# Performance work log

Hardware: AMD Instinct MI355X
Metric: run time of the kernel (lower is better)

Reference implementation:

```python
import jax, jax.numpy as jnp
import numpy as np

B, C_IN, H, W = 4, 64, 512, 512
C_OUT = 64


def _box_sum(x):
    """3x3 box sum with zero padding == applying (A + I) for the 8-connected grid.
    x: [B, H, W, C] -> [B, H, W, C]
    """
    b, h, w, c = x.shape
    xp = jnp.pad(x, ((0, 0), (1, 1), (1, 1), (0, 0)))
    out = jnp.zeros_like(x)
    for i in range(3):
        for j in range(3):
            out = out + xp[:, i:i + h, j:j + w, :]
    return out


def setup_inputs() -> dict:
    key = jax.random.key(0)
    k1, k2 = jax.random.split(key)
    x = jax.random.normal(k1, (B, C_IN, H, W), dtype=jnp.float32)
    weight = jax.random.normal(k2, (1, C_IN, C_OUT), dtype=jnp.float32)
    return {"x": x, "weight": weight}


def reference(x, weight):
    b, c, h, w = x.shape
    o = weight.shape[-1]
    # x.permute(0,2,3,1).reshape(B, H*W, C) -> keep as [B,H,W,C] grid
    x1 = jnp.transpose(x, (0, 2, 3, 1))
    # xw = x1 @ weight  (weight has leading broadcast dim of 1)
    xw = jnp.einsum('bhwc,co->bhwo', x1, weight[0])
    # Normalized adjacency D^{-1/2}(A+I)D^{-1/2} as a 3x3 stencil:
    # deg = number of 8-neighbors + self-loop (9 interior, 6 edge, 4 corner)
    deg = _box_sum(jnp.ones((1, h, w, 1), dtype=x.dtype))
    dinv = 1.0 / jnp.sqrt(deg)  # no isolated nodes on a grid
    y = dinv * _box_sum(dinv * xw)  # [B,H,W,O]
    # out.permute(0,2,1).reshape(B, O, W, H); with H==W this equals plain NCHW
    out = jnp.transpose(y, (0, 3, 1, 2)).reshape(b, o, w, h)
    return out
```

## Files before the change

kernel.cpp:

```cpp
#include <hip/hip_runtime.h>

#define HH 512
#define WWID 512
#define CIN 64
#define COUT 64
#define TH 8
#define TW 32

__device__ __forceinline__ float edge_rsqrt(int y, int n) {
  int r = 1 + (y > 0 ? 1 : 0) + (y < n - 1 ? 1 : 0);
  return __frsqrt_rn((float)r);
}

__global__ __launch_bounds__(256, 4)
void gcn_fused(const float* __restrict__ x, const float* __restrict__ wgt,
               float* __restrict__ out) {
  __shared__ __align__(16) float ts[4][TH * TW];

  const int t  = threadIdx.x;
  const int g  = t & 63;
  const int og = __builtin_amdgcn_readfirstlane(t >> 6);
  const int b  = blockIdx.z;
  const int h0 = blockIdx.y * TH;
  const int w0 = blockIdx.x * TW;
  const int row = g >> 3;
  const int cg  = g & 7;
  const int h = h0 + row;
  const int w = w0 + cg * 4;

  float srh[3]; int hi[3];
#pragma unroll
  for (int i = 0; i < 3; ++i) {
    int y = h - 1 + i;
    bool v = (y >= 0) && (y < HH);
    srh[i] = v ? edge_rsqrt(y, HH) : 0.0f;
    hi[i] = v ? y : h;
  }
  float srw[6];
#pragma unroll
  for (int j = 0; j < 6; ++j) {
    int xw = w - 1 + j;
    bool v = (xw >= 0) && (xw < WWID);
    srw[j] = v ? edge_rsqrt(xw, WWID) : 0.0f;
  }
  const int wl = (w > 0) ? (w - 1) : w;
  const int wr = (w + 4 < WWID) ? (w + 4) : w;
  const float dp0 = srh[1] * srw[1];
  const float dp1 = srh[1] * srw[2];
  const float dp2 = srh[1] * srw[3];
  const float dp3 = srh[1] * srw[4];

  float4 acc[16];
#pragma unroll
  for (int j = 0; j < 16; ++j) acc[j] = make_float4(0.f, 0.f, 0.f, 0.f);

  const size_t plane = (size_t)HH * WWID;
  const float* xb = x + (size_t)b * CIN * plane;

  float lv[3], rv[3]; float4 mv[3];
  {
    const float* xp = xb + (size_t)og * plane;
#pragma unroll
    for (int i = 0; i < 3; ++i) {
      const float* rp = xp + (size_t)hi[i] * WWID;
      lv[i] = rp[wl];
      mv[i] = *(const float4*)(rp + w);
      rv[i] = rp[wr];
    }
  }

  for (int ci = 0; ci < 16; ++ci) {
    float t0 = 0.f, t1 = 0.f, t2 = 0.f, t3 = 0.f;
#pragma unroll
    for (int i = 0; i < 3; ++i) {
      float m0 = lv[i] * srw[0];
      float m1 = mv[i].x * srw[1];
      float m2 = mv[i].y * srw[2];
      float m3 = mv[i].z * srw[3];
      float m4 = mv[i].w * srw[4];
      float m5 = rv[i] * srw[5];
      t0 += srh[i] * (m0 + m1 + m2);
      t1 += srh[i] * (m1 + m2 + m3);
      t2 += srh[i] * (m2 + m3 + m4);
      t3 += srh[i] * (m3 + m4 + m5);
    }
    __syncthreads();
    *(float4*)&ts[og][4 * g] = make_float4(t0, t1, t2, t3);
    __syncthreads();

    if (ci < 15) {
      const float* xp = xb + (size_t)((ci + 1) * 4 + og) * plane;
#pragma unroll
      for (int i = 0; i < 3; ++i) {
        const float* rp = xp + (size_t)hi[i] * WWID;
        lv[i] = rp[wl];
        mv[i] = *(const float4*)(rp + w);
        rv[i] = rp[wr];
      }
    }

#pragma unroll
    for (int cc = 0; cc < 4; ++cc) {
      float4 tv = *(const float4*)&ts[cc][4 * g];
      const float* wp = wgt + (ci * 4 + cc) * COUT + og * 16;
#pragma unroll
      for (int j = 0; j < 16; ++j) {
        float wj = wp[j];
        acc[j].x += tv.x * wj;
        acc[j].y += tv.y * wj;
        acc[j].z += tv.z * wj;
        acc[j].w += tv.w * wj;
      }
    }
  }

  float* ob = out + (size_t)b * COUT * plane + (size_t)h * WWID + w;
#pragma unroll
  for (int j = 0; j < 16; ++j) {
    int o = og * 16 + j;
    float4 r;
    r.x = acc[j].x * dp0;
    r.y = acc[j].y * dp1;
    r.z = acc[j].z * dp2;
    r.w = acc[j].w * dp3;
    *(float4*)(ob + (size_t)o * plane) = r;
  }
}

extern "C" void kernel_launch(void* const* d_in, const int* in_sizes, int n_in,
                              void* d_out, int out_size, void* d_ws, size_t ws_size,
                              hipStream_t stream) {
  const float* x = (const float*)d_in[0];
  const float* wgt = (const float*)d_in[1];
  float* out = (float*)d_out;
  dim3 grid(WWID / TW, HH / TH, 4);
  gcn_fused<<<grid, dim3(256), 0, stream>>>(x, wgt, out);
}
```

Before: 521.8 us.

## Process two channels per wave per step with double-buffered LDS and nontemporal stores

Measured after the change: 684.5 us. +31.2%, slower.

```diff
diff --git a/kernel.cpp b/kernel.cpp
--- a/kernel.cpp
+++ b/kernel.cpp
@@ -7,15 +7,17 @@
 #define TH 8
 #define TW 32
 
+typedef float fx4 __attribute__((ext_vector_type(4)));
+
 __device__ __forceinline__ float edge_rsqrt(int y, int n) {
   int r = 1 + (y > 0 ? 1 : 0) + (y < n - 1 ? 1 : 0);
   return __frsqrt_rn((float)r);
 }
 
-__global__ __launch_bounds__(256, 4)
+__global__ __launch_bounds__(256, 3)
 void gcn_fused(const float* __restrict__ x, const float* __restrict__ wgt,
                float* __restrict__ out) {
-  __shared__ __align__(16) float ts[4][TH * TW];
+  __shared__ __align__(16) float ts[2][8][TH * TW];
 
   const int t  = threadIdx.x;
   const int g  = t & 63;
@@ -45,10 +47,6 @@
   }
   const int wl = (w > 0) ? (w - 1) : w;
   const int wr = (w + 4 < WWID) ? (w + 4) : w;
-  const float dp0 = srh[1] * srw[1];
-  const float dp1 = srh[1] * srw[2];
-  const float dp2 = srh[1] * srw[3];
-  const float dp3 = srh[1] * srw[4];
 
   float4 acc[16];
 #pragma unroll
@@ -57,52 +55,54 @@
   const size_t plane = (size_t)HH * WWID;
   const float* xb = x + (size_t)b * CIN * plane;
 
-  float lv[3], rv[3]; float4 mv[3];
-  {
-    const float* xp = xb + (size_t)og * plane;
+  float lv[2][3], rv[2][3]; float4 mv[2][3];
+#pragma unroll
+  for (int k = 0; k < 2; ++k) {
+    const float* xp = xb + (size_t)(og * 2 + k) * plane;
 #pragma unroll
     for (int i = 0; i < 3; ++i) {
       const float* rp = xp + (size_t)hi[i] * WWID;
-      lv[i] = rp[wl];
-      mv[i] = *(const float4*)(rp + w);
-      rv[i] = rp[wr];
+      lv[k][i] = rp[wl];
+      mv[k][i] = *(const float4*)(rp + w);
+      rv[k][i] = rp[wr];
     }
   }
 
-  for (int ci = 0; ci < 16; ++ci) {
-    float t0 = 0.f, t1 = 0.f, t2 = 0.f, t3 = 0.f;
+  for (int p = 0; p < 8; ++p) {
 #pragma unroll
-    for (int i = 0; i < 3; ++i) {
-      float m0 = lv[i] * srw[0];
-      float m1 = mv[i].x * srw[1];
-      float m2 = mv[i].y * srw[2];
-      float m3 = mv[i].z * srw[3];
-      float m4 = mv[i].w * srw[4];
-      float m5 = rv[i] * srw[5];
-      t0 += srh[i] * (m0 + m1 + m2);
-      t1 += srh[i] * (m1 + m2 + m3);
-      t2 += srh[i] * (m2 + m3 + m4);
-      t3 += srh[i] * (m3 + m4 + m5);
+    for (int k = 0; k < 2; ++k) {
+      float vs0 = lv[k][0]   * srh[0] + lv[k][1]   * srh[1] + lv[k][2]   * srh[2];
+      float vs1 = mv[k][0].x * srh[0] + mv[k][1].x * srh[1] + mv[k][2].x * srh[2];
+      float vs2 = mv[k][0].y * srh[0] + mv[k][1].y * srh[1] + mv[k][2].y * srh[2];
+      float vs3 = mv[k][0].z * srh[0] + mv[k][1].z * srh[1] + mv[k][2].z * srh[2];
+      float vs4 = mv[k][0].w * srh[0] + mv[k][1].w * srh[1] + mv[k][2].w * srh[2];
+      float vs5 = rv[k][0]   * srh[0] + rv[k][1]   * srh[1] + rv[k][2]   * srh[2];
+      float t0 = srw[0] * vs0 + srw[1] * vs1 + srw[2] * vs2;
+      float t1 = srw[1] * vs1 + srw[2] * vs2 + srw[3] * vs3;
+      float t2 = srw[2] * vs2 + srw[3] * vs3 + srw[4] * vs4;
+      float t3 = srw[3] * vs3 + srw[4] * vs4 + srw[5] * vs5;
+      *(float4*)&ts[p & 1][og * 2 + k][4 * g] = make_float4(t0, t1, t2, t3);
     }
     __syncthreads();
-    *(float4*)&ts[og][4 * g] = make_float4(t0, t1, t2, t3);
-    __syncthreads();
 
-    if (ci < 15) {
-      const float* xp = xb + (size_t)((ci + 1) * 4 + og) * plane;
+    if (p < 7) {
 #pragma unroll
-      for (int i = 0; i < 3; ++i) {
-        const float* rp = xp + (size_t)hi[i] * WWID;
-        lv[i] = rp[wl];
-        mv[i] = *(const float4*)(rp + w);
-        rv[i] = rp[wr];
+      for (int k = 0; k < 2; ++k) {
+        const float* xp = xb + (size_t)((p + 1) * 8 + og * 2 + k) * plane;
+#pragma unroll
+        for (int i = 0; i < 3; ++i) {
+          const float* rp = xp + (size_t)hi[i] * WWID;
+          lv[k][i] = rp[wl];
+          mv[k][i] = *(const float4*)(rp + w);
+          rv[k][i] = rp[wr];
+        }
       }
     }
 
 #pragma unroll
-    for (int cc = 0; cc < 4; ++cc) {
-      float4 tv = *(const float4*)&ts[cc][4 * g];
-      const float* wp = wgt + (ci * 4 + cc) * COUT + og * 16;
+    for (int cc = 0; cc < 8; ++cc) {
+      float4 tv = *(const float4*)&ts[p & 1][cc][4 * g];
+      const float* wp = wgt + (size_t)(p * 8 + cc) * COUT + og * 16;
 #pragma unroll
       for (int j = 0; j < 16; ++j) {
         float wj = wp[j];
@@ -114,16 +114,19 @@
     }
   }
 
+  const float dp0 = srh[1] * srw[1];
+  const float dp1 = srh[1] * srw[2];
+  const float dp2 = srh[1] * srw[3];
+  const float dp3 = srh[1] * srw[4];
   float* ob = out + (size_t)b * COUT * plane + (size_t)h * WWID + w;
 #pragma unroll
   for (int j = 0; j < 16; ++j) {
-    int o = og * 16 + j;
-    float4 r;
+    fx4 r;
     r.x = acc[j].x * dp0;
     r.y = acc[j].y * dp1;
     r.z = acc[j].z * dp2;
     r.w = acc[j].w * dp3;
-    *(float4*)(ob + (size_t)o * plane) = r;
+    __builtin_nontemporal_store(r, (fx4*)(ob + (size_t)(og * 16 + j) * plane));
   }
 }
 
```
